# Kernel optimization log

Hardware: AMD Instinct MI355X
Metric: run time of the kernel (lower is better)

## Reference

```python
import jax, jax.numpy as jnp
import numpy as np

NEG_SLOPE = 0.2

def setup_inputs() -> dict:
    key = jax.random.key(0)
    k1, k2, k3, k4, k5 = jax.random.split(key, 5)
    B, N, Fin, Fout, H = 4, 2048, 256, 128, 4
    h = jax.random.normal(k1, (B, N, Fin), dtype=jnp.float32)
    adj = jax.random.randint(k2, (N, N), 0, 2, dtype=jnp.int32)
    W_w = jax.random.normal(k3, (Fout, Fin), dtype=jnp.float32) * (1.414 / np.sqrt(Fin))
    W_b = jax.random.normal(k4, (Fout,), dtype=jnp.float32) * 0.01
    attn_w = jax.random.normal(k5, (H, 2 * Fout), dtype=jnp.float32) * (1.414 / np.sqrt(2 * Fout))
    return {"h": h, "adj": adj, "W_w": W_w, "W_b": W_b, "attn_w": attn_w}

def reference(h, adj, W_w, W_b, attn_w):
    Fout = W_w.shape[0]
    # Wh: [B, N, Fout]
    Wh = jnp.einsum('bnf,of->bno', h, W_w) + W_b
    a_left = attn_w[:, :Fout]   # [H, Fout]
    a_right = attn_w[:, Fout:]  # [H, Fout]
    e_left = jnp.einsum('bno,ho->bhn', Wh, a_left)   # [B, H, N]
    e_right = jnp.einsum('bno,ho->bhn', Wh, a_right)  # [B, H, N]
    # additive broadcast score: [B, H, N, N]
    e = e_left[:, :, :, None] + e_right[:, :, None, :]
    e = jnp.where(e > 0, e, NEG_SLOPE * e)  # LeakyReLU(0.2)
    mask = (adj == 0)[None, None, :, :]     # [1,1,N,N] broadcast over B,H
    e = jnp.where(mask, -jnp.inf, e)
    attn = jax.nn.softmax(e, axis=-1)
    attn = jnp.where(jnp.isnan(attn), 0.0, attn)
    # h_prime: [B, H, N, Fout]
    h_prime = jnp.einsum('bhij,bjo->bhio', attn, Wh)
    out = jnp.mean(h_prime, axis=1)
    return jax.nn.relu(out)
```

## Files before the change

kernel.cpp:

```cpp
#include <hip/hip_runtime.h>
#include <stdint.h>

#define BB 4
#define NN 2048
#define FIN 256
#define FOUT 128
#define NH 4
#define NEG_SLOPE 0.2f

typedef short bf16x8 __attribute__((ext_vector_type(8)));
typedef unsigned short u16x8 __attribute__((ext_vector_type(8)));
typedef float f32x4 __attribute__((ext_vector_type(4)));
typedef unsigned long long u64;

__device__ inline float b2f(unsigned short u) {
    union { unsigned int i; float f; } x; x.i = ((unsigned int)u) << 16; return x.f;
}
__device__ inline unsigned short f2b(float f) {
    union { float f; unsigned int i; } x; x.f = f;
    unsigned int r = x.i + 0x7fffu + ((x.i >> 16) & 1u);
    return (unsigned short)(r >> 16);
}
__device__ inline unsigned short f2b_fast(float f) {
    union { float f; unsigned int i; } x; x.f = f;
    return (unsigned short)((x.i + 0x8000u) >> 16);
}

__global__ __launch_bounds__(256) void k0_prep(const float* __restrict__ Ww,
                                               unsigned short* __restrict__ Whi,
                                               unsigned short* __restrict__ Wlo,
                                               const int* __restrict__ adj,
                                               u64* __restrict__ mask) {
    int bid = blockIdx.x;
    if (bid < 128) {
        int idx = bid * 256 + threadIdx.x;
        float v = Ww[idx];
        unsigned short hb = f2b(v);
        Whi[idx] = hb;
        Wlo[idx] = f2b(v - b2f(hb));
    } else {
        int row = bid - 128;
        int wave = threadIdx.x >> 6, lane = threadIdx.x & 63;
        #pragma unroll
        for (int it = 0; it < 8; ++it) {
            int w = it * 4 + wave;
            int j = w * 64 + lane;
            u64 m = __ballot(adj[(size_t)row * NN + j] != 0);
            if (lane == 0) mask[row * 32 + w] = m;
        }
    }
}

__global__ __launch_bounds__(256) void k1_wh(
    const float* __restrict__ h, const unsigned short* __restrict__ Whi,
    const unsigned short* __restrict__ Wlo, const float* __restrict__ Wb,
    const float* __restrict__ attw, unsigned short* __restrict__ WhT,
    float2* __restrict__ ELpair, float2* __restrict__ ERf) {
    __shared__ unsigned short Ahi[16][264];
    __shared__ unsigned short Alo[16][264];
    __shared__ float whs[16][132];
    int t = threadIdx.x;
    int b = blockIdx.x >> 7;
    int n0 = (blockIdx.x & 127) * 16;
    {
        int r = t >> 4, c = (t & 15) * 16;
        const float* hp = h + ((size_t)(b * NN + n0 + r)) * FIN + c;
        u16x8 hi0, hi1, lo0, lo1;
        #pragma unroll
        for (int q = 0; q < 4; ++q) {
            float4 v = *(const float4*)(hp + q * 4);
            float vv[4] = {v.x, v.y, v.z, v.w};
            #pragma unroll
            for (int e = 0; e < 4; ++e) {
                int idx = q * 4 + e;
                unsigned short hb = f2b(vv[e]);
                unsigned short lb = f2b(vv[e] - b2f(hb));
                if (idx < 8) { hi0[idx] = (short)hb; lo0[idx] = (short)lb; }
                else         { hi1[idx - 8] = (short)hb; lo1[idx - 8] = (short)lb; }
            }
        }
        *(u16x8*)&Ahi[r][c] = *(u16x8*)&hi0;
        *(u16x8*)&Ahi[r][c + 8] = *(u16x8*)&hi1;
        *(u16x8*)&Alo[r][c] = *(u16x8*)&lo0;
        *(u16x8*)&Alo[r][c + 8] = *(u16x8*)&lo1;
    }
    __syncthreads();
    int lane = t & 63, wv = t >> 6;
    int m = lane & 15, quad = lane >> 4;
    int o0 = wv * 32;
    f32x4 acc0 = {0.f, 0.f, 0.f, 0.f}, acc1 = {0.f, 0.f, 0.f, 0.f};
    const unsigned short* wh0 = Whi + (size_t)(o0 + m) * FIN;
    const unsigned short* wl0 = Wlo + (size_t)(o0 + m) * FIN;
    const unsigned short* wh1 = Whi + (size_t)(o0 + 16 + m) * FIN;
    const unsigned short* wl1 = Wlo + (size_t)(o0 + 16 + m) * FIN;
    #pragma unroll
    for (int ks = 0; ks < 8; ++ks) {
        int ko = ks * 32 + quad * 8;
        bf16x8 ahi = *(bf16x8*)&Ahi[m][ko];
        bf16x8 alo = *(bf16x8*)&Alo[m][ko];
        bf16x8 bh0 = *(const bf16x8*)(wh0 + ko);
        bf16x8 bl0 = *(const bf16x8*)(wl0 + ko);
        bf16x8 bh1 = *(const bf16x8*)(wh1 + ko);
        bf16x8 bl1 = *(const bf16x8*)(wl1 + ko);
        acc0 = __builtin_amdgcn_mfma_f32_16x16x32_bf16(ahi, bh0, acc0, 0, 0, 0);
        acc0 = __builtin_amdgcn_mfma_f32_16x16x32_bf16(ahi, bl0, acc0, 0, 0, 0);
        acc0 = __builtin_amdgcn_mfma_f32_16x16x32_bf16(alo, bh0, acc0, 0, 0, 0);
        acc1 = __builtin_amdgcn_mfma_f32_16x16x32_bf16(ahi, bh1, acc1, 0, 0, 0);
        acc1 = __builtin_amdgcn_mfma_f32_16x16x32_bf16(ahi, bl1, acc1, 0, 0, 0);
        acc1 = __builtin_amdgcn_mfma_f32_16x16x32_bf16(alo, bh1, acc1, 0, 0, 0);
    }
    float bias0 = Wb[o0 + m], bias1 = Wb[o0 + 16 + m];
    #pragma unroll
    for (int reg = 0; reg < 4; ++reg) {
        int row = quad * 4 + reg;
        whs[row][o0 + m] = acc0[reg] + bias0;
        whs[row][o0 + 16 + m] = acc1[reg] + bias1;
    }
    __syncthreads();
    {
        int o = t >> 1, half = t & 1;
        u16x8 v8;
        #pragma unroll
        for (int r = 0; r < 8; ++r) v8[r] = (short)f2b(whs[half * 8 + r][o]);
        *(u16x8*)(WhT + (size_t)(b * FOUT + o) * NN + n0 + half * 8) = v8;
    }
    {
        int outi = t >> 1, half = t & 1;
        int i = outi >> 3, d = outi & 7, hh = d & 3, side = d >> 2;
        const float* arow = attw + hh * (2 * FOUT) + side * FOUT + half * 64;
        float s = 0.f;
        #pragma unroll 8
        for (int k = 0; k < 64; ++k) s = fmaf(whs[i][half * 64 + k], arow[k], s);
        s += __shfl_xor(s, 1);
        if (half == 0) {
            float p = __expf(s), n = __expf(NEG_SLOPE * s);
            if (side == 0) {
                ELpair[(size_t)(b * NH + hh) * NN + n0 + i] = make_float2(p, n);
            } else {
                ERf[((size_t)b * NN + n0 + i) * NH + hh] = make_float2(p, n);
            }
        }
    }
}

__global__ __launch_bounds__(256) void kstat_t(
    const float2* __restrict__ ERf, const float2* __restrict__ ELpair,
    const u64* __restrict__ mask, float* __restrict__ sPartT) {
    int lane = threadIdx.x & 63, b = threadIdx.x >> 6;
    int i = blockIdx.x * 64 + lane;
    int j0 = blockIdx.y * 64;
    u64 mw = mask[(size_t)i * 32 + (j0 >> 6)];
    float elp[NH], eln[NH], acc[NH];
    #pragma unroll
    for (int hh = 0; hh < NH; ++hh) {
        float2 e2 = ELpair[(size_t)(b * NH + hh) * NN + i];
        elp[hh] = e2.x; eln[hh] = e2.y; acc[hh] = 0.f;
    }
    const float4* erb = (const float4*)(ERf + ((size_t)b * NN + j0) * NH);
    #pragma unroll 8
    for (int jj = 0; jj < 64; ++jj) {
        float4 e0 = erb[jj * 2];
        float4 e1 = erb[jj * 2 + 1];
        bool bit = (mw >> jj) & 1ull;
        float m0 = fmaxf(elp[0] * e0.x, eln[0] * e0.y);
        float m1 = fmaxf(elp[1] * e0.z, eln[1] * e0.w);
        float m2 = fmaxf(elp[2] * e1.x, eln[2] * e1.y);
        float m3 = fmaxf(elp[3] * e1.z, eln[3] * e1.w);
        acc[0] += bit ? m0 : 0.f;
        acc[1] += bit ? m1 : 0.f;
        acc[2] += bit ? m2 : 0.f;
        acc[3] += bit ? m3 : 0.f;
    }
    #pragma unroll
    for (int hh = 0; hh < NH; ++hh)
        sPartT[(((size_t)blockIdx.y * BB + b) * NH + hh) * NN + i] = acc[hh];
}

__global__ __launch_bounds__(512, 4) void k2b_mfma(
    const unsigned short* __restrict__ WhT, const float2* __restrict__ ERf,
    const float2* __restrict__ ELpair, const float* __restrict__ sPartT,
    const u64* __restrict__ mask, float* __restrict__ P) {
    __shared__ unsigned short wt[64][264];
    __shared__ u64 mws[64][8];
    __shared__ float elsc_s[64][8];
    int t = threadIdx.x;
    int b = blockIdx.y, i0 = blockIdx.x * 64, jq = blockIdx.z;
    int lane = t & 63, wv = t >> 6;
    int m = lane & 15, quad = lane >> 4;
    if (t < 256) {
        int li = t & 63, hh = t >> 6;
        float s = 0.f;
        #pragma unroll
        for (int jp = 0; jp < 32; ++jp)
            s += sPartT[(((size_t)jp * BB + b) * NH + hh) * NN + i0 + li];
        float iv = (s > 0.f) ? 0.25f / s : 0.f;
        float2 e2 = ELpair[(size_t)(b * NH + hh) * NN + i0 + li];
        elsc_s[li][hh * 2]     = e2.x * iv;
        elsc_s[li][hh * 2 + 1] = e2.y * iv;
    }
    {
        int r = t >> 3, wp = t & 7;
        mws[r][wp] = mask[(size_t)(i0 + r) * 32 + jq * 8 + wp];
    }
    int r0 = wv * 8;
    int o0 = wv * 16;
    const unsigned short* bp = WhT + (size_t)(b * FOUT + o0 + m) * NN + jq * 512;
    f32x4 acc[4];
    #pragma unroll
    for (int k = 0; k < 4; ++k) acc[k] = (f32x4){0.f, 0.f, 0.f, 0.f};

    for (int ch = 0; ch < 2; ++ch) {
        int j0 = ch * 256;
        __syncthreads();
        bf16x8 bfr[8];
        #pragma unroll
        for (int ks = 0; ks < 8; ++ks)
            bfr[ks] = *(const bf16x8*)(bp + j0 + ks * 32 + quad * 8);
        float erp[4][4], ern[4][4];
        #pragma unroll
        for (int q = 0; q < 4; ++q) {
            int jg = jq * 512 + j0 + q * 64 + lane;
            const float4* ef = (const float4*)(ERf + ((size_t)b * NN + jg) * NH);
            float4 e0 = ef[0], e1 = ef[1];
            erp[q][0] = e0.x; ern[q][0] = e0.y;
            erp[q][1] = e0.z; ern[q][1] = e0.w;
            erp[q][2] = e1.x; ern[q][2] = e1.y;
            erp[q][3] = e1.z; ern[q][3] = e1.w;
        }
        #pragma unroll
        for (int r = 0; r < 8; ++r) {
            int ir = r0 + r;
            float4 c0 = *(float4*)&elsc_s[ir][0];
            float4 c1 = *(float4*)&elsc_s[ir][4];
            u64 mwq[4] = {mws[ir][ch * 4 + 0], mws[ir][ch * 4 + 1],
                          mws[ir][ch * 4 + 2], mws[ir][ch * 4 + 3]};
            #pragma unroll
            for (int q = 0; q < 4; ++q) {
                float p = fmaxf(c0.x * erp[q][0], c0.y * ern[q][0]);
                p += fmaxf(c0.z * erp[q][1], c0.w * ern[q][1]);
                p += fmaxf(c1.x * erp[q][2], c1.y * ern[q][2]);
                p += fmaxf(c1.z * erp[q][3], c1.w * ern[q][3]);
                wt[ir][q * 64 + lane] = ((mwq[q] >> lane) & 1ull) ? f2b_fast(p) : 0;
            }
        }
        __syncthreads();
        #pragma unroll
        for (int isub = 0; isub < 4; ++isub) {
            #pragma unroll
            for (int ks = 0; ks < 8; ++ks) {
                bf16x8 a = *(bf16x8*)&wt[isub * 16 + m][ks * 32 + quad * 8];
                acc[isub] = __builtin_amdgcn_mfma_f32_16x16x32_bf16(a, bfr[ks], acc[isub], 0, 0, 0);
            }
        }
    }
    float* pb = P + (((size_t)jq * BB + b) * NN + i0) * FOUT;
    #pragma unroll
    for (int isub = 0; isub < 4; ++isub) {
        #pragma unroll
        for (int reg = 0; reg < 4; ++reg) {
            int row = isub * 16 + quad * 4 + reg;
            pb[(size_t)row * FOUT + o0 + m] = acc[isub][reg];
        }
    }
}

__global__ __launch_bounds__(256) void k3_relu(const float* __restrict__ P,
                                               float* __restrict__ out) {
    int idx = blockIdx.x * 256 + threadIdx.x;
    const int slab = BB * NN * FOUT / 4;
    float4 a = ((const float4*)P)[idx];
    float4 c1 = ((const float4*)P)[idx + slab];
    float4 c2 = ((const float4*)P)[idx + 2 * slab];
    float4 c3 = ((const float4*)P)[idx + 3 * slab];
    a.x = fmaxf(a.x + c1.x + c2.x + c3.x, 0.f);
    a.y = fmaxf(a.y + c1.y + c2.y + c3.y, 0.f);
    a.z = fmaxf(a.z + c1.z + c2.z + c3.z, 0.f);
    a.w = fmaxf(a.w + c1.w + c2.w + c3.w, 0.f);
    ((float4*)out)[idx] = a;
}

extern "C" void kernel_launch(void* const* d_in, const int* in_sizes, int n_in,
                              void* d_out, int out_size, void* d_ws, size_t ws_size,
                              hipStream_t stream) {
    const float* h    = (const float*)d_in[0];
    const int* adj    = (const int*)d_in[1];
    const float* Ww   = (const float*)d_in[2];
    const float* Wb   = (const float*)d_in[3];
    const float* attw = (const float*)d_in[4];
    float* out = (float*)d_out;
    char* ws = (char*)d_ws;
    unsigned short* Whi = (unsigned short*)(ws);
    unsigned short* Wlo = (unsigned short*)(ws + 65536);
    unsigned short* WhT = (unsigned short*)(ws + 131072);
    float2*       ELpair = (float2*)(ws + 2228224);
    float2*       ERf    = (float2*)(ws + 2490368);
    u64*          mask   = (u64*)(ws + 2752512);
    float*        sPartT = (float*)(ws + 3276800);
    float*        P      = (float*)(ws + 7471104);

    k0_prep<<<dim3(128 + NN), dim3(256), 0, stream>>>(Ww, Whi, Wlo, adj, mask);
    k1_wh<<<dim3(BB * NN / 16), dim3(256), 0, stream>>>(h, Whi, Wlo, Wb, attw,
                                                        WhT, ELpair, ERf);
    kstat_t<<<dim3(NN / 64, NN / 64), dim3(256), 0, stream>>>(ERf, ELpair, mask, sPartT);
    k2b_mfma<<<dim3(NN / 64, BB, 4), dim3(512), 0, stream>>>(WhT, ERf, ELpair,
                                                             sPartT, mask, P);
    k3_relu<<<dim3(BB * NN * FOUT / 1024), dim3(256), 0, stream>>>(P, out);
}
```

Measured before the change: 128.9 us.

## Fuse softmax-denominator pass, attention matmul and ReLU into one kernel

```diff
diff --git a/kernel.cpp b/kernel.cpp
--- a/kernel.cpp
+++ b/kernel.cpp
@@ -143,73 +143,67 @@
     }
 }
 
-__global__ __launch_bounds__(256) void kstat_t(
-    const float2* __restrict__ ERf, const float2* __restrict__ ELpair,
-    const u64* __restrict__ mask, float* __restrict__ sPartT) {
-    int lane = threadIdx.x & 63, b = threadIdx.x >> 6;
-    int i = blockIdx.x * 64 + lane;
-    int j0 = blockIdx.y * 64;
-    u64 mw = mask[(size_t)i * 32 + (j0 >> 6)];
-    float elp[NH], eln[NH], acc[NH];
-    #pragma unroll
-    for (int hh = 0; hh < NH; ++hh) {
-        float2 e2 = ELpair[(size_t)(b * NH + hh) * NN + i];
-        elp[hh] = e2.x; eln[hh] = e2.y; acc[hh] = 0.f;
-    }
-    const float4* erb = (const float4*)(ERf + ((size_t)b * NN + j0) * NH);
-    #pragma unroll 8
-    for (int jj = 0; jj < 64; ++jj) {
-        float4 e0 = erb[jj * 2];
-        float4 e1 = erb[jj * 2 + 1];
-        bool bit = (mw >> jj) & 1ull;
-        float m0 = fmaxf(elp[0] * e0.x, eln[0] * e0.y);
-        float m1 = fmaxf(elp[1] * e0.z, eln[1] * e0.w);
-        float m2 = fmaxf(elp[2] * e1.x, eln[2] * e1.y);
-        float m3 = fmaxf(elp[3] * e1.z, eln[3] * e1.w);
-        acc[0] += bit ? m0 : 0.f;
-        acc[1] += bit ? m1 : 0.f;
-        acc[2] += bit ? m2 : 0.f;
-        acc[3] += bit ? m3 : 0.f;
-    }
-    #pragma unroll
-    for (int hh = 0; hh < NH; ++hh)
-        sPartT[(((size_t)blockIdx.y * BB + b) * NH + hh) * NN + i] = acc[hh];
-}
-
-__global__ __launch_bounds__(512, 4) void k2b_mfma(
+__global__ __launch_bounds__(512, 4) void k2_fused(
     const unsigned short* __restrict__ WhT, const float2* __restrict__ ERf,
-    const float2* __restrict__ ELpair, const float* __restrict__ sPartT,
-    const u64* __restrict__ mask, float* __restrict__ P) {
-    __shared__ unsigned short wt[64][264];
-    __shared__ u64 mws[64][8];
-    __shared__ float elsc_s[64][8];
+    const float2* __restrict__ ELpair, const u64* __restrict__ mask,
+    float* __restrict__ out) {
+    __shared__ unsigned short wt[16][264];
+    __shared__ u64 mws[16][32];
+    __shared__ float part[32][16][NH];
+    __shared__ float elsc_s[16][8];
     int t = threadIdx.x;
-    int b = blockIdx.y, i0 = blockIdx.x * 64, jq = blockIdx.z;
+    int b = blockIdx.y, i0 = blockIdx.x * 16;
     int lane = t & 63, wv = t >> 6;
     int m = lane & 15, quad = lane >> 4;
-    if (t < 256) {
-        int li = t & 63, hh = t >> 6;
+
+    {
+        int r = t >> 5, w = t & 31;
+        mws[r][w] = mask[(size_t)(i0 + r) * 32 + w];
+    }
+    __syncthreads();
+
+    {
+        int i = t & 15, strip = t >> 4;
+        float elp[NH], eln[NH], acc[NH];
+        #pragma unroll
+        for (int hh = 0; hh < NH; ++hh) {
+            float2 e2 = ELpair[(size_t)(b * NH + hh) * NN + i0 + i];
+            elp[hh] = e2.x; eln[hh] = e2.y; acc[hh] = 0.f;
+        }
+        u64 mw = mws[i][strip];
+        const float4* erb = (const float4*)(ERf + ((size_t)b * NN + strip * 64) * NH);
+        #pragma unroll 8
+        for (int jj = 0; jj < 64; ++jj) {
+            float4 e0 = erb[jj * 2];
+            float4 e1 = erb[jj * 2 + 1];
+            bool bit = (mw >> jj) & 1ull;
+            float m0 = fmaxf(elp[0] * e0.x, eln[0] * e0.y);
+            float m1 = fmaxf(elp[1] * e0.z, eln[1] * e0.w);
+            float m2 = fmaxf(elp[2] * e1.x, eln[2] * e1.y);
+            float m3 = fmaxf(elp[3] * e1.z, eln[3] * e1.w);
+            acc[0] += bit ? m0 : 0.f;
+            acc[1] += bit ? m1 : 0.f;
+            acc[2] += bit ? m2 : 0.f;
+            acc[3] += bit ? m3 : 0.f;
+        }
+        #pragma unroll
+        for (int hh = 0; hh < NH; ++hh) part[strip][i][hh] = acc[hh];
+    }
+    __syncthreads();
+    if (t < 64) {
+        int i = t >> 2, hh = t & 3;
         float s = 0.f;
         #pragma unroll
-        for (int jp = 0; jp < 32; ++jp)
-            s += sPartT[(((size_t)jp * BB + b) * NH + hh) * NN + i0 + li];
+        for (int st = 0; st < 32; ++st) s += part[st][i][hh];
         float iv = (s > 0.f) ? 0.25f / s : 0.f;
-        float2 e2 = ELpair[(size_t)(b * NH + hh) * NN + i0 + li];
-        elsc_s[li][hh * 2]     = e2.x * iv;
-        elsc_s[li][hh * 2 + 1] = e2.y * iv;
-    }
-    {
-        int r = t >> 3, wp = t & 7;
-        mws[r][wp] = mask[(size_t)(i0 + r) * 32 + jq * 8 + wp];
-    }
-    int r0 = wv * 8;
-    int o0 = wv * 16;
-    const unsigned short* bp = WhT + (size_t)(b * FOUT + o0 + m) * NN + jq * 512;
-    f32x4 acc[4];
-    #pragma unroll
-    for (int k = 0; k < 4; ++k) acc[k] = (f32x4){0.f, 0.f, 0.f, 0.f};
-
-    for (int ch = 0; ch < 2; ++ch) {
+        float2 e2 = ELpair[(size_t)(b * NH + hh) * NN + i0 + i];
+        elsc_s[i][hh * 2]     = e2.x * iv;
+        elsc_s[i][hh * 2 + 1] = e2.y * iv;
+    }
+
+    const unsigned short* bp = WhT + (size_t)(b * FOUT + wv * 16 + m) * NN;
+    f32x4 acc = {0.f, 0.f, 0.f, 0.f};
+    for (int ch = 0; ch < 8; ++ch) {
         int j0 = ch * 256;
         __syncthreads();
         bf16x8 bfr[8];
@@ -219,7 +213,7 @@
         float erp[4][4], ern[4][4];
         #pragma unroll
         for (int q = 0; q < 4; ++q) {
-            int jg = jq * 512 + j0 + q * 64 + lane;
+            int jg = j0 + q * 64 + lane;
             const float4* ef = (const float4*)(ERf + ((size_t)b * NN + jg) * NH);
             float4 e0 = ef[0], e1 = ef[1];
             erp[q][0] = e0.x; ern[q][0] = e0.y;
@@ -228,55 +222,33 @@
             erp[q][3] = e1.z; ern[q][3] = e1.w;
         }
         #pragma unroll
-        for (int r = 0; r < 8; ++r) {
-            int ir = r0 + r;
+        for (int r = 0; r < 2; ++r) {
+            int ir = wv * 2 + r;
             float4 c0 = *(float4*)&elsc_s[ir][0];
             float4 c1 = *(float4*)&elsc_s[ir][4];
-            u64 mwq[4] = {mws[ir][ch * 4 + 0], mws[ir][ch * 4 + 1],
-                          mws[ir][ch * 4 + 2], mws[ir][ch * 4 + 3]};
             #pragma unroll
             for (int q = 0; q < 4; ++q) {
                 float p = fmaxf(c0.x * erp[q][0], c0.y * ern[q][0]);
                 p += fmaxf(c0.z * erp[q][1], c0.w * ern[q][1]);
                 p += fmaxf(c1.x * erp[q][2], c1.y * ern[q][2]);
                 p += fmaxf(c1.z * erp[q][3], c1.w * ern[q][3]);
-                wt[ir][q * 64 + lane] = ((mwq[q] >> lane) & 1ull) ? f2b_fast(p) : 0;
+                wt[ir][q * 64 + lane] =
+                    ((mws[ir][ch * 4 + q] >> lane) & 1ull) ? f2b_fast(p) : 0;
             }
         }
         __syncthreads();
         #pragma unroll
-        for (int isub = 0; isub < 4; ++isub) {
-            #pragma unroll
-            for (int ks = 0; ks < 8; ++ks) {
-                bf16x8 a = *(bf16x8*)&wt[isub * 16 + m][ks * 32 + quad * 8];
-                acc[isub] = __builtin_amdgcn_mfma_f32_16x16x32_bf16(a, bfr[ks], acc[isub], 0, 0, 0);
-            }
-        }
-    }
-    float* pb = P + (((size_t)jq * BB + b) * NN + i0) * FOUT;
+        for (int ks = 0; ks < 8; ++ks) {
+            bf16x8 a = *(bf16x8*)&wt[m][ks * 32 + quad * 8];
+            acc = __builtin_amdgcn_mfma_f32_16x16x32_bf16(a, bfr[ks], acc, 0, 0, 0);
+        }
+    }
     #pragma unroll
-    for (int isub = 0; isub < 4; ++isub) {
-        #pragma unroll
-        for (int reg = 0; reg < 4; ++reg) {
-            int row = isub * 16 + quad * 4 + reg;
-            pb[(size_t)row * FOUT + o0 + m] = acc[isub][reg];
-        }
-    }
-}
-
-__global__ __launch_bounds__(256) void k3_relu(const float* __restrict__ P,
-                                               float* __restrict__ out) {
-    int idx = blockIdx.x * 256 + threadIdx.x;
-    const int slab = BB * NN * FOUT / 4;
-    float4 a = ((const float4*)P)[idx];
-    float4 c1 = ((const float4*)P)[idx + slab];
-    float4 c2 = ((const float4*)P)[idx + 2 * slab];
-    float4 c3 = ((const float4*)P)[idx + 3 * slab];
-    a.x = fmaxf(a.x + c1.x + c2.x + c3.x, 0.f);
-    a.y = fmaxf(a.y + c1.y + c2.y + c3.y, 0.f);
-    a.z = fmaxf(a.z + c1.z + c2.z + c3.z, 0.f);
-    a.w = fmaxf(a.w + c1.w + c2.w + c3.w, 0.f);
-    ((float4*)out)[idx] = a;
+    for (int reg = 0; reg < 4; ++reg) {
+        int row = quad * 4 + reg;
+        out[((size_t)b * NN + i0 + row) * FOUT + wv * 16 + m] =
+            fmaxf(acc[reg], 0.f);
+    }
 }
 
 extern "C" void kernel_launch(void* const* d_in, const int* in_sizes, int n_in,
@@ -295,14 +267,10 @@
     float2*       ELpair = (float2*)(ws + 2228224);
     float2*       ERf    = (float2*)(ws + 2490368);
     u64*          mask   = (u64*)(ws + 2752512);
-    float*        sPartT = (float*)(ws + 3276800);
-    float*        P      = (float*)(ws + 7471104);
 
     k0_prep<<<dim3(128 + NN), dim3(256), 0, stream>>>(Ww, Whi, Wlo, adj, mask);
     k1_wh<<<dim3(BB * NN / 16), dim3(256), 0, stream>>>(h, Whi, Wlo, Wb, attw,
                                                         WhT, ELpair, ERf);
-    kstat_t<<<dim3(NN / 64, NN / 64), dim3(256), 0, stream>>>(ERf, ELpair, mask, sPartT);
-    k2b_mfma<<<dim3(NN / 64, BB, 4), dim3(512), 0, stream>>>(WhT, ERf, ELpair,
-                                                             sPartT, mask, P);
-    k3_relu<<<dim3(BB * NN * FOUT / 1024), dim3(256), 0, stream>>>(P, out);
-}
+    k2_fused<<<dim3(NN / 16, BB), dim3(512), 0, stream>>>(WhT, ERf, ELpair,
+                                                          mask, out);
+}
```

After: 149.9 us. 16.3% more time.
